# Optimization experiments

Measured on AMD Instinct MI355X. Metric: run time of the kernel, lower is better.

## Reference

```python
import jax, jax.numpy as jnp
import numpy as np
from functools import partial

TAU = 2.0
V_TH = 1.0
ALPHA = 2.0  # spikingjelly surrogate.ATan default alpha
EPS = 1e-5   # nn.LayerNorm default eps

@jax.custom_vjp
def atan_spike(v):
    # Heaviside forward; ATan surrogate gradient in bwd.
    return (v >= 0.0).astype(v.dtype)

def _atan_fwd(v):
    return atan_spike(v), v

def _atan_bwd(v, g):
    sg = (ALPHA / 2.0) / (1.0 + (jnp.pi / 2.0 * ALPHA * v) ** 2)
    return (g * sg,)

atan_spike.defvjp(_atan_fwd, _atan_bwd)

def lif_multi_step(x):
    # x: [B, T, H]; LIF with decay_input=True, v_reset=0 (hard reset), detach_reset=True.
    xt = jnp.swapaxes(x, 0, 1)  # [T, B, H]
    v0 = jnp.zeros(x.shape[:1] + x.shape[2:], dtype=x.dtype)  # reset_net per call
    def step(v, x_t):
        v = v + (x_t - v) / TAU            # charge
        s = atan_spike(v - V_TH)           # fire (surrogate grad)
        v = v * (1.0 - jax.lax.stop_gradient(s))  # hard reset to 0, detached spike
        return v, s
    _, spikes = jax.lax.scan(step, v0, xt)
    return jnp.swapaxes(spikes, 0, 1)  # [B, T, H]

def layer_norm(x, gamma, beta):
    mu = jnp.mean(x, axis=-1, keepdims=True)
    var = jnp.mean((x - mu) ** 2, axis=-1, keepdims=True)
    return (x - mu) * jax.lax.rsqrt(var + EPS) * gamma + beta

def setup_inputs() -> dict:
    key = jax.random.key(0)
    ks = jax.random.split(key, 5)
    B, T, D, H = 64, 1024, 256, 512
    x = jax.random.normal(ks[0], (B, T, D), dtype=jnp.float32)
    sc1 = 1.0 / np.sqrt(D)
    sc2 = 1.0 / np.sqrt(H)
    W1 = jax.random.uniform(ks[1], (H, D), jnp.float32, -sc1, sc1)
    b1 = jax.random.uniform(ks[2], (H,), jnp.float32, -sc1, sc1)
    W2 = jax.random.uniform(ks[3], (D, H), jnp.float32, -sc2, sc2)
    b2 = jax.random.uniform(ks[4], (D,), jnp.float32, -sc2, sc2)
    g1 = jnp.ones((H,), jnp.float32); be1 = jnp.zeros((H,), jnp.float32)
    g2 = jnp.ones((D,), jnp.float32); be2 = jnp.zeros((D,), jnp.float32)
    return {"x": x, "W1": W1, "b1": b1, "g1": g1, "be1": be1,
            "W2": W2, "b2": b2, "g2": g2, "be2": be2}

def reference(x, W1, b1, g1, be1, W2, b2, g2, be2):
    residual = x
    h = jnp.einsum('btd,hd->bth', x, W1) + b1   # fc1
    h = layer_norm(h, g1, be1)                   # norm1
    h = lif_multi_step(h)                        # lif1 (dropout = identity, eval)
    y = jnp.einsum('bth,dh->btd', h, W2) + b2    # fc2
    y = layer_norm(y, g2, be2)                   # norm2
    y = lif_multi_step(y)                        # lif2
    return residual + y
```

## Files before the change

### kernel.cpp

```cpp
#include <hip/hip_runtime.h>

typedef int   v4i __attribute__((ext_vector_type(4)));
typedef int  v16i __attribute__((ext_vector_type(16)));
typedef float v4f __attribute__((ext_vector_type(4)));

#define TT 1024
#define DD 256
#define HH 512
#define CB 32
#define CM (CB*TT)

static __device__ __forceinline__ double shfl_xor_d(double x, int m) {
    union { double d; int u[2]; } a; a.d = x;
    a.u[0] = __shfl_xor(a.u[0], m);
    a.u[1] = __shfl_xor(a.u[1], m);
    return a.d;
}

__global__ __launch_bounds__(256) void prep_w_k(const float* __restrict__ W1,
                                                const float* __restrict__ W2,
                                                signed char* __restrict__ W1p,
                                                signed char* __restrict__ W2p) {
    int i = blockIdx.x * 256 + threadIdx.x;
    {
        double a = (double)W1[i];
        double inv = 1024.0, s = 1.0 / 1024.0;
#pragma unroll
        for (int p = 0; p < 5; ++p) {
            int d = (int)(a * inv);
            a -= d * s;
            W1p[(size_t)p * 131072 + i] = (signed char)d;
            inv *= 128.0; s *= (1.0 / 128.0);
        }
    }
    {
        double a = (double)W2[i];
        double inv = 1024.0, s = 1.0 / 1024.0;
#pragma unroll
        for (int p = 0; p < 5; ++p) {
            int d = (int)(a * inv);
            a -= d * s;
            W2p[(size_t)p * 131072 + i] = (signed char)d;
            inv *= 128.0; s *= (1.0 / 128.0);
        }
    }
}

__global__ __launch_bounds__(256) void split_x_k(const float* __restrict__ xc,
                                                 signed char* __restrict__ Xp) {
    int gid = blockIdx.x * 256 + threadIdx.x;
    int e0 = gid * 4;
    v4f xv = *(const v4f*)(xc + e0);
    int dg[4][5];
#pragma unroll
    for (int e = 0; e < 4; ++e) {
        float a = xv[e];
        float inv = 8.0f, s = 0.125f;
#pragma unroll
        for (int p = 0; p < 5; ++p) {
            int d = (int)(a * inv);
            a -= (float)d * s;
            dg[e][p] = d;
            inv *= 128.0f; s *= (1.0f / 128.0f);
        }
    }
#pragma unroll
    for (int p = 0; p < 5; ++p) {
        int pk = (dg[0][p] & 255) | ((dg[1][p] & 255) << 8) |
                 ((dg[2][p] & 255) << 16) | ((dg[3][p] & 255) << 24);
        *(int*)(Xp + (size_t)p * ((size_t)CM * 256) + e0) = pk;
    }
}

__global__ __launch_bounds__(256, 2) void gemm1_i8(
    const signed char* __restrict__ Xp, const signed char* __restrict__ W1p,
    const float* __restrict__ b1, double* __restrict__ Hn,
    double* __restrict__ PS1w, double* __restrict__ PQ1w) {
    __shared__ signed char Asm[5 * 8192];

    const int tid = threadIdx.x;
    const int wn = tid >> 6, lane = tid & 63, lrow = lane & 31, lhalf = lane >> 5;
    const int ch = blockIdx.x;
    const int m0 = blockIdx.y * 32;

    {
        const int r = tid >> 3, k0 = (tid & 7) * 32;
        const int swz = (r & 15) << 4;
#pragma unroll
        for (int p = 0; p < 5; ++p) {
            const signed char* sp = Xp + (size_t)p * ((size_t)CM * 256) +
                                    (size_t)(m0 + r) * 256 + k0;
            v4i v0 = *(const v4i*)(sp);
            v4i v1 = *(const v4i*)(sp + 16);
            *(v4i*)&Asm[p * 8192 + r * 256 + (k0 ^ swz)] = v0;
            *(v4i*)&Asm[p * 8192 + r * 256 + ((k0 + 16) ^ swz)] = v1;
        }
    }

    const int colbase = ch * 256 + wn * 32 + lrow;
    const signed char* bptr = W1p + (size_t)colbase * 256 + lhalf * 16;

    v4i bf[3][5];
#pragma unroll
    for (int s = 0; s < 2; ++s)
#pragma unroll
        for (int j = 0; j < 5; ++j)
            bf[s][j] = *(const v4i*)(bptr + (size_t)j * 131072 +
                                     (s >> 3) * 32768 + (s & 7) * 32);

    v16i acc[5];

    __syncthreads();

    const double scl[5] = {0x1p-13, 0x1p-20, 0x1p-27, 0x1p-34, 0x1p-41};
    const int aswz = (lrow & 15) << 4;

#pragma unroll
    for (int p = 0; p < 2; ++p) {
#pragma unroll
        for (int g = 0; g < 5; ++g)
#pragma unroll
            for (int r = 0; r < 16; ++r) acc[g][r] = 0;
#pragma unroll
        for (int ksl = 0; ksl < 8; ++ksl) {
            const int s = p * 8 + ksl;
            if (s + 2 < 16) {
                const int s2 = s + 2;
#pragma unroll
                for (int j = 0; j < 5; ++j)
                    bf[s2 % 3][j] = *(const v4i*)(bptr + (size_t)j * 131072 +
                                                  (s2 >> 3) * 32768 + (s2 & 7) * 32);
            }
            v4i af[5];
#pragma unroll
            for (int i = 0; i < 5; ++i)
                af[i] = *(const v4i*)&Asm[i * 8192 + lrow * 256 +
                                          ((ksl * 32 + lhalf * 16) ^ aswz)];
#pragma unroll
            for (int j = 0; j < 5; ++j)
#pragma unroll
                for (int i = 0; i + j < 5; ++i)
                    acc[i + j] = __builtin_amdgcn_mfma_i32_32x32x32_i8(
                        af[i], bf[s % 3][j], acc[i + j], 0, 0, 0);
        }
        const int col = colbase + p * 128;
        const double bcol = (double)b1[col];
        const size_t qbase = (size_t)((ch * 2 + p) * 4 + wn) * CM + m0;
#pragma unroll
        for (int r = 0; r < 16; ++r) {
            double t = 0.0;
#pragma unroll
            for (int g = 0; g < 5; ++g) t = fma((double)acc[g][r], scl[g], t);
            const double hr = t + bcol;
            const int crow = (r & 3) + 8 * (r >> 2) + 4 * lhalf;
            Hn[(size_t)(m0 + crow) * HH + col] = hr;
            double ps = hr, pq = hr * hr;
#pragma unroll
            for (int m = 1; m < 32; m <<= 1) {
                ps += shfl_xor_d(ps, m);
                pq += shfl_xor_d(pq, m);
            }
            if (lrow == 0) {
                PS1w[qbase + crow] = ps;
                PQ1w[qbase + crow] = pq;
            }
        }
    }
}

__global__ __launch_bounds__(256) void stats1_fin(const double* __restrict__ PS1w,
                                                  const double* __restrict__ PQ1w,
                                                  double2* __restrict__ MUIV1) {
    int row = blockIdx.x * 256 + threadIdx.x;
    double S = 0.0, Q = 0.0;
#pragma unroll
    for (int q = 0; q < 16; ++q) {
        S += PS1w[(size_t)q * CM + row];
        Q += PQ1w[(size_t)q * CM + row];
    }
    double mu = S * (1.0 / 512.0);
    double var = Q * (1.0 / 512.0) - mu * mu;
    MUIV1[row] = make_double2(mu, 1.0 / sqrt(var + 1e-5));
}

__global__ __launch_bounds__(64) void lif1_k(const double* __restrict__ Hn,
                                             const double2* __restrict__ MUIV,
                                             const float* __restrict__ g1,
                                             const float* __restrict__ be1,
                                             signed char* __restrict__ S) {
    const int b = blockIdx.x >> 3;
    const int h = (blockIdx.x & 7) * 64 + threadIdx.x;
    __shared__ double2 MI[4][16];
    const double* src = Hn + (size_t)b * TT * HH + h;
    signed char* dst = S + (size_t)b * TT * HH + h;
    const double gg = (double)g1[h], be = (double)be1[h];
    if (threadIdx.x < 48)
        MI[threadIdx.x >> 4][threadIdx.x & 15] = MUIV[(size_t)b * TT + threadIdx.x];
    double buf[4][16];
#pragma unroll
    for (int gq = 0; gq < 3; ++gq)
#pragma unroll
        for (int t = 0; t < 16; ++t)
            buf[gq][t] = src[(size_t)(gq * 16 + t) * HH];
    __syncthreads();
    double v = 0.0;
    for (int g4 = 0; g4 < 64; g4 += 4) {
#pragma unroll
        for (int u = 0; u < 4; ++u) {
            const int g = g4 + u;
            __syncthreads();
            if (g + 3 < 64) {
                if (threadIdx.x < 16)
                    MI[(g + 3) & 3][threadIdx.x] =
                        MUIV[(size_t)b * TT + (g + 3) * 16 + threadIdx.x];
#pragma unroll
                for (int t = 0; t < 16; ++t)
                    buf[(u + 3) & 3][t] = src[(size_t)((g + 3) * 16 + t) * HH];
            }
#pragma unroll
            for (int t = 0; t < 16; ++t) {
                const double2 mi = MI[g & 3][t];
                const double x = (buf[u][t] - mi.x) * mi.y * gg + be;
                v += (x - v) * 0.5;
                const bool sp = (v >= 1.0);
                dst[(size_t)(g * 16 + t) * HH] = sp ? 1 : 0;
                if (sp) v = 0.0;
            }
        }
    }
}

__global__ __launch_bounds__(256, 2) void gemm2_i8(
    const signed char* __restrict__ Sb, const signed char* __restrict__ W2p,
    const float* __restrict__ b2, double* __restrict__ Yn,
    double2* __restrict__ MUIV2) {
    __shared__ signed char Asm[32 * 512];
    __shared__ double RSs[2][4][32], RQs[2][4][32];

    const int tid = threadIdx.x;
    const int wn = tid >> 6, lane = tid & 63, lrow = lane & 31, lhalf = lane >> 5;
    const int m0 = blockIdx.x * 32;

    {
        const int r = tid >> 3, k0 = (tid & 7) * 64;
        const signed char* sp = Sb + (size_t)(m0 + r) * HH + k0;
        const int swz = (r & 15) << 4;
#pragma unroll
        for (int q = 0; q < 4; ++q) {
            v4i v = *(const v4i*)(sp + q * 16);
            *(v4i*)&Asm[r * 512 + ((k0 + q * 16) ^ swz)] = v;
        }
    }

    const signed char* bptr = W2p + (size_t)(wn * 32 + lrow) * 512 + lhalf * 16;

    v4i bf[3][5];
#pragma unroll
    for (int s = 0; s < 2; ++s)
#pragma unroll
        for (int j = 0; j < 5; ++j)
            bf[s][j] = *(const v4i*)(bptr + (size_t)j * 131072 +
                                     (s >> 4) * 65536 + (s & 15) * 32);

    v16i acc[5];

    __syncthreads();

    const double scl[5] = {0x1p-10, 0x1p-17, 0x1p-24, 0x1p-31, 0x1p-38};
    const int aswz = (lrow & 15) << 4;

#pragma unroll
    for (int p = 0; p < 2; ++p) {
#pragma unroll
        for (int g = 0; g < 5; ++g)
#pragma unroll
            for (int r = 0; r < 16; ++r) acc[g][r] = 0;
#pragma unroll
        for (int ksl = 0; ksl < 16; ++ksl) {
            const int s = p * 16 + ksl;
            if (s + 2 < 32) {
                const int s2 = s + 2;
#pragma unroll
                for (int j = 0; j < 5; ++j)
                    bf[s2 % 3][j] = *(const v4i*)(bptr + (size_t)j * 131072 +
                                                  (s2 >> 4) * 65536 + (s2 & 15) * 32);
            }
            v4i a = *(const v4i*)&Asm[lrow * 512 + ((ksl * 32 + lhalf * 16) ^ aswz)];
#pragma unroll
            for (int j = 0; j < 5; ++j)
                acc[j] = __builtin_amdgcn_mfma_i32_32x32x32_i8(a, bf[s % 3][j], acc[j], 0, 0, 0);
        }
        const int col = p * 128 + wn * 32 + lrow;
        const double bcol = (double)b2[col];
#pragma unroll
        for (int r = 0; r < 16; ++r) {
            double t = 0.0;
#pragma unroll
            for (int g = 0; g < 5; ++g) t = fma((double)acc[g][r], scl[g], t);
            const double yr = t + bcol;
            const int crow = (r & 3) + 8 * (r >> 2) + 4 * lhalf;
            Yn[(size_t)(m0 + crow) * DD + col] = yr;
            double ps = yr, pq = yr * yr;
#pragma unroll
            for (int m = 1; m < 32; m <<= 1) {
                ps += shfl_xor_d(ps, m);
                pq += shfl_xor_d(pq, m);
            }
            if (lrow == 0) {
                RSs[p][wn][crow] = ps;
                RQs[p][wn][crow] = pq;
            }
        }
    }
    __syncthreads();
    if (tid < 32) {
        double Ssum = 0.0, Qsum = 0.0;
#pragma unroll
        for (int p = 0; p < 2; ++p)
#pragma unroll
            for (int w = 0; w < 4; ++w) { Ssum += RSs[p][w][tid]; Qsum += RQs[p][w][tid]; }
        const double mu = Ssum * (1.0 / 256.0);
        const double var = Qsum * (1.0 / 256.0) - mu * mu;
        MUIV2[m0 + tid] = make_double2(mu, 1.0 / sqrt(var + 1e-5));
    }
}

__global__ __launch_bounds__(64) void lif2_k(const double* __restrict__ Yn,
                                             const double2* __restrict__ MUIV,
                                             const float* __restrict__ g2,
                                             const float* __restrict__ be2,
                                             const float* __restrict__ X,
                                             float* __restrict__ out) {
    const int b = blockIdx.x >> 2;
    const int d = (blockIdx.x & 3) * 64 + threadIdx.x;
    __shared__ double2 MI[4][16];
    const double* src = Yn + (size_t)b * TT * DD + d;
    const float* xs = X + (size_t)b * TT * DD + d;
    float* dst = out + (size_t)b * TT * DD + d;
    const double gg = (double)g2[d], be = (double)be2[d];
    if (threadIdx.x < 48)
        MI[threadIdx.x >> 4][threadIdx.x & 15] = MUIV[(size_t)b * TT + threadIdx.x];
    double bufy[4][16];
    float bufx[4][16];
#pragma unroll
    for (int gq = 0; gq < 3; ++gq)
#pragma unroll
        for (int t = 0; t < 16; ++t) {
            bufy[gq][t] = src[(size_t)(gq * 16 + t) * DD];
            bufx[gq][t] = xs[(size_t)(gq * 16 + t) * DD];
        }
    __syncthreads();
    double v = 0.0;
    for (int g4 = 0; g4 < 64; g4 += 4) {
#pragma unroll
        for (int u = 0; u < 4; ++u) {
            const int g = g4 + u;
            __syncthreads();
            if (g + 3 < 64) {
                if (threadIdx.x < 16)
                    MI[(g + 3) & 3][threadIdx.x] =
                        MUIV[(size_t)b * TT + (g + 3) * 16 + threadIdx.x];
#pragma unroll
                for (int t = 0; t < 16; ++t) {
                    bufy[(u + 3) & 3][t] = src[(size_t)((g + 3) * 16 + t) * DD];
                    bufx[(u + 3) & 3][t] = xs[(size_t)((g + 3) * 16 + t) * DD];
                }
            }
#pragma unroll
            for (int t = 0; t < 16; ++t) {
                const double2 mi = MI[g & 3][t];
                const double x = (bufy[u][t] - mi.x) * mi.y * gg + be;
                v += (x - v) * 0.5;
                const bool sp = (v >= 1.0);
                __builtin_nontemporal_store(bufx[u][t] + (sp ? 1.0f : 0.0f),
                                            &dst[(size_t)(g * 16 + t) * DD]);
                if (sp) v = 0.0;
            }
        }
    }
}

extern "C" void kernel_launch(void* const* d_in, const int* in_sizes, int n_in,
                              void* d_out, int out_size, void* d_ws, size_t ws_size,
                              hipStream_t stream) {
    const float* x   = (const float*)d_in[0];
    const float* W1  = (const float*)d_in[1];
    const float* b1  = (const float*)d_in[2];
    const float* g1  = (const float*)d_in[3];
    const float* be1 = (const float*)d_in[4];
    const float* W2  = (const float*)d_in[5];
    const float* b2  = (const float*)d_in[6];
    const float* g2  = (const float*)d_in[7];
    const float* be2 = (const float*)d_in[8];
    float* out = (float*)d_out;

    char* ws = (char*)d_ws;
    signed char* W1p = (signed char*)ws;
    signed char* W2p = (signed char*)(ws + (1ull << 20));
    double*      Hn  = (double*)(ws + (2ull << 20));
    signed char* Sb  = (signed char*)(ws + (130ull << 20));
    double*      Yn  = (double*)(ws + (146ull << 20));
    signed char* Xp    = (signed char*)(ws + (146ull << 20));
    double*      PS1w  = (double*)(ws + (186ull << 20));
    double*      PQ1w  = (double*)(ws + (190ull << 20));
    double2*     MUIV1 = (double2*)(ws + (194ull << 20));
    double2*     MUIV2 = (double2*)(ws + (210ull << 20));

    prep_w_k<<<dim3(512), dim3(256), 0, stream>>>(W1, W2, W1p, W2p);

    for (int c = 0; c < 2; ++c) {
        const float* xc = x + (size_t)c * CM * DD;
        float* outc = out + (size_t)c * CM * DD;
        split_x_k<<<dim3(8192), dim3(256), 0, stream>>>(xc, Xp);
        gemm1_i8<<<dim3(2, CM / 32), dim3(256), 0, stream>>>(Xp, W1p, b1, Hn, PS1w, PQ1w);
        stats1_fin<<<dim3(CM / 256), dim3(256), 0, stream>>>(PS1w, PQ1w, MUIV1);
        lif1_k<<<dim3(CB * 8), dim3(64), 0, stream>>>(Hn, MUIV1, g1, be1, Sb);
        gemm2_i8<<<dim3(CM / 32), dim3(256), 0, stream>>>(Sb, W2p, b2, Yn, MUIV2);
        lif2_k<<<dim3(CB * 4), dim3(64), 0, stream>>>(Yn, MUIV2, g2, be2, xc, outc);
    }
}
```

Before: 715.2 us.

## Fuse x digit split into gemm1 and switch GEMMs to 16x16x64 int8 MFMA

The separate split_x_k kernel is removed. gemm1 now loads fp32 x directly and decomposes it into five int8 digit planes in shared memory, so the 5-plane int8 staging buffer no longer makes a round trip through global memory. Both GEMMs move from 32x32x32 to 16x16x64 int8 MFMA with a 2x2 wave layout. Each block now covers all output columns in a loop over phases, and gemm1 becomes a one-dimensional grid. gemm2's in-block LayerNorm stat reduction is replaced by partial sums plus a new stats2_fin kernel, and workspace buffers are remapped. The cost is one extra launch and redundant digit splitting, since each gemm1 block now handles all 512 columns.

```diff
diff --git a/kernel.cpp b/kernel.cpp
--- a/kernel.cpp
+++ b/kernel.cpp
@@ -1,7 +1,6 @@
 #include <hip/hip_runtime.h>
 
 typedef int   v4i __attribute__((ext_vector_type(4)));
-typedef int  v16i __attribute__((ext_vector_type(16)));
 typedef float v4f __attribute__((ext_vector_type(4)));
 
 #define TT 1024
@@ -46,123 +45,122 @@
     }
 }
 
-__global__ __launch_bounds__(256) void split_x_k(const float* __restrict__ xc,
-                                                 signed char* __restrict__ Xp) {
-    int gid = blockIdx.x * 256 + threadIdx.x;
-    int e0 = gid * 4;
-    v4f xv = *(const v4f*)(xc + e0);
-    int dg[4][5];
-#pragma unroll
-    for (int e = 0; e < 4; ++e) {
-        float a = xv[e];
-        float inv = 8.0f, s = 0.125f;
-#pragma unroll
-        for (int p = 0; p < 5; ++p) {
-            int d = (int)(a * inv);
-            a -= (float)d * s;
-            dg[e][p] = d;
-            inv *= 128.0f; s *= (1.0f / 128.0f);
-        }
-    }
-#pragma unroll
-    for (int p = 0; p < 5; ++p) {
-        int pk = (dg[0][p] & 255) | ((dg[1][p] & 255) << 8) |
-                 ((dg[2][p] & 255) << 16) | ((dg[3][p] & 255) << 24);
-        *(int*)(Xp + (size_t)p * ((size_t)CM * 256) + e0) = pk;
-    }
-}
-
 __global__ __launch_bounds__(256, 2) void gemm1_i8(
-    const signed char* __restrict__ Xp, const signed char* __restrict__ W1p,
+    const float* __restrict__ X, const signed char* __restrict__ W1p,
     const float* __restrict__ b1, double* __restrict__ Hn,
     double* __restrict__ PS1w, double* __restrict__ PQ1w) {
     __shared__ signed char Asm[5 * 8192];
 
     const int tid = threadIdx.x;
-    const int wn = tid >> 6, lane = tid & 63, lrow = lane & 31, lhalf = lane >> 5;
-    const int ch = blockIdx.x;
-    const int m0 = blockIdx.y * 32;
+    const int wave = tid >> 6, lane = tid & 63;
+    const int wm = wave >> 1, wn = wave & 1;
+    const int lcol = lane & 15, lq = lane >> 4;
+    const int m0 = blockIdx.x * 32;
 
     {
         const int r = tid >> 3, k0 = (tid & 7) * 32;
+        const float* xp = X + (size_t)(m0 + r) * DD + k0;
         const int swz = (r & 15) << 4;
 #pragma unroll
-        for (int p = 0; p < 5; ++p) {
-            const signed char* sp = Xp + (size_t)p * ((size_t)CM * 256) +
-                                    (size_t)(m0 + r) * 256 + k0;
-            v4i v0 = *(const v4i*)(sp);
-            v4i v1 = *(const v4i*)(sp + 16);
-            *(v4i*)&Asm[p * 8192 + r * 256 + (k0 ^ swz)] = v0;
-            *(v4i*)&Asm[p * 8192 + r * 256 + ((k0 + 16) ^ swz)] = v1;
-        }
-    }
-
-    const int colbase = ch * 256 + wn * 32 + lrow;
-    const signed char* bptr = W1p + (size_t)colbase * 256 + lhalf * 16;
-
-    v4i bf[3][5];
-#pragma unroll
-    for (int s = 0; s < 2; ++s)
-#pragma unroll
-        for (int j = 0; j < 5; ++j)
-            bf[s][j] = *(const v4i*)(bptr + (size_t)j * 131072 +
-                                     (s >> 3) * 32768 + (s & 7) * 32);
-
-    v16i acc[5];
+        for (int half = 0; half < 2; ++half) {
+            float xe[16];
+#pragma unroll
+            for (int q = 0; q < 4; ++q)
+                *(v4f*)(xe + q * 4) = *(const v4f*)(xp + half * 16 + q * 4);
+            int pk[5][4];
+#pragma unroll
+            for (int q = 0; q < 4; ++q)
+#pragma unroll
+                for (int e = 0; e < 4; ++e) {
+                    float a = xe[q * 4 + e];
+                    float inv = 8.0f, s = 0.125f;
+#pragma unroll
+                    for (int p = 0; p < 5; ++p) {
+                        int dg = (int)(a * inv);
+                        a -= (float)dg * s;
+                        int byte = (dg & 255) << (8 * e);
+                        if (e == 0) pk[p][q] = byte; else pk[p][q] |= byte;
+                        inv *= 128.0f; s *= (1.0f / 128.0f);
+                    }
+                }
+#pragma unroll
+            for (int p = 0; p < 5; ++p)
+                *(v4i*)&Asm[p * 8192 + r * 256 + ((k0 + half * 16) ^ swz)] =
+                    *(const v4i*)&pk[p][0];
+        }
+    }
+
+    const signed char* bptr = W1p + (size_t)(wn * 16 + lcol) * 256 + lq * 16;
+
+    v4i bf[2][5];
+#pragma unroll
+    for (int j = 0; j < 5; ++j)
+        bf[0][j] = *(const v4i*)(bptr + (size_t)j * 131072);
 
     __syncthreads();
 
     const double scl[5] = {0x1p-13, 0x1p-20, 0x1p-27, 0x1p-34, 0x1p-41};
-    const int aswz = (lrow & 15) << 4;
-
-#pragma unroll
-    for (int p = 0; p < 2; ++p) {
+    const int arow = wm * 16 + lcol;
+    const int abase = arow * 256;
+    const int aswz = lcol << 4;
+
+#pragma unroll 1
+    for (int ph = 0; ph < 16; ++ph) {
+        v4i acc[5];
 #pragma unroll
         for (int g = 0; g < 5; ++g)
 #pragma unroll
-            for (int r = 0; r < 16; ++r) acc[g][r] = 0;
-#pragma unroll
-        for (int ksl = 0; ksl < 8; ++ksl) {
-            const int s = p * 8 + ksl;
-            if (s + 2 < 16) {
-                const int s2 = s + 2;
+            for (int r = 0; r < 4; ++r) acc[g][r] = 0;
+
+#pragma unroll
+        for (int ks = 0; ks < 4; ++ks) {
+            if (ks != 3 || ph != 15) {
+                const int s1 = ph * 4 + ks + 1;
+                const size_t off = (size_t)(s1 >> 2) * 8192 + (size_t)((ks + 1) & 3) * 64;
 #pragma unroll
                 for (int j = 0; j < 5; ++j)
-                    bf[s2 % 3][j] = *(const v4i*)(bptr + (size_t)j * 131072 +
-                                                  (s2 >> 3) * 32768 + (s2 & 7) * 32);
+                    bf[(ks + 1) & 1][j] = *(const v4i*)(bptr + (size_t)j * 131072 + off);
             }
             v4i af[5];
 #pragma unroll
             for (int i = 0; i < 5; ++i)
-                af[i] = *(const v4i*)&Asm[i * 8192 + lrow * 256 +
-                                          ((ksl * 32 + lhalf * 16) ^ aswz)];
+                af[i] = *(const v4i*)&Asm[i * 8192 + abase +
+                                          ((ks * 64 + lq * 16) ^ aswz)];
 #pragma unroll
             for (int j = 0; j < 5; ++j)
 #pragma unroll
                 for (int i = 0; i + j < 5; ++i)
-                    acc[i + j] = __builtin_amdgcn_mfma_i32_32x32x32_i8(
-                        af[i], bf[s % 3][j], acc[i + j], 0, 0, 0);
-        }
-        const int col = colbase + p * 128;
+                    acc[i + j] = __builtin_amdgcn_mfma_i32_16x16x64_i8(
+                        af[i], bf[ks & 1][j], acc[i + j], 0, 0, 0);
+        }
+
+        const int col = ph * 32 + wn * 16 + lcol;
         const double bcol = (double)b1[col];
-        const size_t qbase = (size_t)((ch * 2 + p) * 4 + wn) * CM + m0;
-#pragma unroll
-        for (int r = 0; r < 16; ++r) {
+        double vv[4], ps[4], pq[4];
+#pragma unroll
+        for (int r = 0; r < 4; ++r) {
             double t = 0.0;
 #pragma unroll
             for (int g = 0; g < 5; ++g) t = fma((double)acc[g][r], scl[g], t);
-            const double hr = t + bcol;
-            const int crow = (r & 3) + 8 * (r >> 2) + 4 * lhalf;
-            Hn[(size_t)(m0 + crow) * HH + col] = hr;
-            double ps = hr, pq = hr * hr;
-#pragma unroll
-            for (int m = 1; m < 32; m <<= 1) {
-                ps += shfl_xor_d(ps, m);
-                pq += shfl_xor_d(pq, m);
-            }
-            if (lrow == 0) {
-                PS1w[qbase + crow] = ps;
-                PQ1w[qbase + crow] = pq;
+            vv[r] = t + bcol;
+            ps[r] = vv[r]; pq[r] = vv[r] * vv[r];
+        }
+#pragma unroll
+        for (int m = 1; m < 16; m <<= 1)
+#pragma unroll
+            for (int r = 0; r < 4; ++r) {
+                ps[r] += shfl_xor_d(ps[r], m);
+                pq[r] += shfl_xor_d(pq[r], m);
+            }
+#pragma unroll
+        for (int r = 0; r < 4; ++r)
+            Hn[(size_t)(m0 + wm * 16 + lq * 4 + r) * HH + col] = vv[r];
+        if (lcol == 0) {
+            const size_t qb = (size_t)(ph * 2 + wn) * CM + m0 + wm * 16 + lq * 4;
+#pragma unroll
+            for (int r = 0; r < 4; ++r) {
+                PS1w[qb + r] = ps[r];
+                PQ1w[qb + r] = pq[r];
             }
         }
     }
@@ -174,7 +172,7 @@
     int row = blockIdx.x * 256 + threadIdx.x;
     double S = 0.0, Q = 0.0;
 #pragma unroll
-    for (int q = 0; q < 16; ++q) {
+    for (int q = 0; q < 32; ++q) {
         S += PS1w[(size_t)q * CM + row];
         Q += PQ1w[(size_t)q * CM + row];
     }
@@ -233,12 +231,13 @@
 __global__ __launch_bounds__(256, 2) void gemm2_i8(
     const signed char* __restrict__ Sb, const signed char* __restrict__ W2p,
     const float* __restrict__ b2, double* __restrict__ Yn,
-    double2* __restrict__ MUIV2) {
+    double* __restrict__ PS2w, double* __restrict__ PQ2w) {
     __shared__ signed char Asm[32 * 512];
-    __shared__ double RSs[2][4][32], RQs[2][4][32];
 
     const int tid = threadIdx.x;
-    const int wn = tid >> 6, lane = tid & 63, lrow = lane & 31, lhalf = lane >> 5;
+    const int wave = tid >> 6, lane = tid & 63;
+    const int wm = wave >> 1, wn = wave & 1;
+    const int lcol = lane & 15, lq = lane >> 4;
     const int m0 = blockIdx.x * 32;
 
     {
@@ -252,77 +251,89 @@
         }
     }
 
-    const signed char* bptr = W2p + (size_t)(wn * 32 + lrow) * 512 + lhalf * 16;
-
-    v4i bf[3][5];
-#pragma unroll
-    for (int s = 0; s < 2; ++s)
-#pragma unroll
-        for (int j = 0; j < 5; ++j)
-            bf[s][j] = *(const v4i*)(bptr + (size_t)j * 131072 +
-                                     (s >> 4) * 65536 + (s & 15) * 32);
-
-    v16i acc[5];
+    const signed char* bptr = W2p + (size_t)(wn * 16 + lcol) * 512 + lq * 16;
+
+    v4i bf[2][5];
+#pragma unroll
+    for (int j = 0; j < 5; ++j)
+        bf[0][j] = *(const v4i*)(bptr + (size_t)j * 131072);
 
     __syncthreads();
 
     const double scl[5] = {0x1p-10, 0x1p-17, 0x1p-24, 0x1p-31, 0x1p-38};
-    const int aswz = (lrow & 15) << 4;
-
-#pragma unroll
-    for (int p = 0; p < 2; ++p) {
+    const int arow = wm * 16 + lcol;
+    const int abase = arow * 512;
+    const int aswz = lcol << 4;
+
+#pragma unroll 1
+    for (int ph = 0; ph < 8; ++ph) {
+        v4i acc[5];
 #pragma unroll
         for (int g = 0; g < 5; ++g)
 #pragma unroll
-            for (int r = 0; r < 16; ++r) acc[g][r] = 0;
-#pragma unroll
-        for (int ksl = 0; ksl < 16; ++ksl) {
-            const int s = p * 16 + ksl;
-            if (s + 2 < 32) {
-                const int s2 = s + 2;
+            for (int r = 0; r < 4; ++r) acc[g][r] = 0;
+
+#pragma unroll
+        for (int ks = 0; ks < 8; ++ks) {
+            if (ks != 7 || ph != 7) {
+                const int s1 = ph * 8 + ks + 1;
+                const size_t off = (size_t)(s1 >> 3) * 16384 + (size_t)((ks + 1) & 7) * 64;
 #pragma unroll
                 for (int j = 0; j < 5; ++j)
-                    bf[s2 % 3][j] = *(const v4i*)(bptr + (size_t)j * 131072 +
-                                                  (s2 >> 4) * 65536 + (s2 & 15) * 32);
-            }
-            v4i a = *(const v4i*)&Asm[lrow * 512 + ((ksl * 32 + lhalf * 16) ^ aswz)];
+                    bf[(ks + 1) & 1][j] = *(const v4i*)(bptr + (size_t)j * 131072 + off);
+            }
+            v4i a = *(const v4i*)&Asm[abase + ((ks * 64 + lq * 16) ^ aswz)];
 #pragma unroll
             for (int j = 0; j < 5; ++j)
-                acc[j] = __builtin_amdgcn_mfma_i32_32x32x32_i8(a, bf[s % 3][j], acc[j], 0, 0, 0);
-        }
-        const int col = p * 128 + wn * 32 + lrow;
+                acc[j] = __builtin_amdgcn_mfma_i32_16x16x64_i8(
+                    a, bf[ks & 1][j], acc[j], 0, 0, 0);
+        }
+
+        const int col = ph * 32 + wn * 16 + lcol;
         const double bcol = (double)b2[col];
-#pragma unroll
-        for (int r = 0; r < 16; ++r) {
+        double vv[4], ps[4], pq[4];
+#pragma unroll
+        for (int r = 0; r < 4; ++r) {
             double t = 0.0;
 #pragma unroll
             for (int g = 0; g < 5; ++g) t = fma((double)acc[g][r], scl[g], t);
-            const double yr = t + bcol;
-            const int crow = (r & 3) + 8 * (r >> 2) + 4 * lhalf;
-            Yn[(size_t)(m0 + crow) * DD + col] = yr;
-            double ps = yr, pq = yr * yr;
-#pragma unroll
-            for (int m = 1; m < 32; m <<= 1) {
-                ps += shfl_xor_d(ps, m);
-                pq += shfl_xor_d(pq, m);
-            }
-            if (lrow == 0) {
-                RSs[p][wn][crow] = ps;
-                RQs[p][wn][crow] = pq;
-            }
-        }
-    }
-    __syncthreads();
-    if (tid < 32) {
-        double Ssum = 0.0, Qsum = 0.0;
-#pragma unroll
-        for (int p = 0; p < 2; ++p)
-#pragma unroll
-            for (int w = 0; w < 4; ++w) { Ssum += RSs[p][w][tid]; Qsum += RQs[p][w][tid]; }
-        const double mu = Ssum * (1.0 / 256.0);
-        const double var = Qsum * (1.0 / 256.0) - mu * mu;
-        MUIV2[m0 + tid] = make_double2(mu, 1.0 / sqrt(var + 1e-5));
-    }
+            vv[r] = t + bcol;
+            ps[r] = vv[r]; pq[r] = vv[r] * vv[r];
+        }
+#pragma unroll
+        for (int m = 1; m < 16; m <<= 1)
+#pragma unroll
+            for (int r = 0; r < 4; ++r) {
+                ps[r] += shfl_xor_d(ps[r], m);
+                pq[r] += shfl_xor_d(pq[r], m);
+            }
+#pragma unroll
+        for (int r = 0; r < 4; ++r)
+            Yn[(size_t)(m0 + wm * 16 + lq * 4 + r) * DD + col] = vv[r];
+        if (lcol == 0) {
+            const size_t qb = (size_t)(ph * 2 + wn) * CM + m0 + wm * 16 + lq * 4;
+#pragma unroll
+            for (int r = 0; r < 4; ++r) {
+                PS2w[qb + r] = ps[r];
+                PQ2w[qb + r] = pq[r];
+            }
+        }
+    }
+}
+
+__global__ __launch_bounds__(256) void stats2_fin(const double* __restrict__ PS2w,
+                                                  const double* __restrict__ PQ2w,
+                                                  double2* __restrict__ MUIV2) {
+    int row = blockIdx.x * 256 + threadIdx.x;
+    double S = 0.0, Q = 0.0;
+#pragma unroll
+    for (int q = 0; q < 16; ++q) {
+        S += PS2w[(size_t)q * CM + row];
+        Q += PQ2w[(size_t)q * CM + row];
+    }
+    double mu = S * (1.0 / 256.0);
+    double var = Q * (1.0 / 256.0) - mu * mu;
+    MUIV2[row] = make_double2(mu, 1.0 / sqrt(var + 1e-5));
 }
 
 __global__ __launch_bounds__(64) void lif2_k(const double* __restrict__ Yn,
@@ -400,22 +411,23 @@
     double*      Hn  = (double*)(ws + (2ull << 20));
     signed char* Sb  = (signed char*)(ws + (130ull << 20));
     double*      Yn  = (double*)(ws + (146ull << 20));
-    signed char* Xp    = (signed char*)(ws + (146ull << 20));
-    double*      PS1w  = (double*)(ws + (186ull << 20));
-    double*      PQ1w  = (double*)(ws + (190ull << 20));
-    double2*     MUIV1 = (double2*)(ws + (194ull << 20));
-    double2*     MUIV2 = (double2*)(ws + (210ull << 20));
+    double*      PS1w  = (double*)(ws + (146ull << 20));
+    double*      PQ1w  = (double*)(ws + (154ull << 20));
+    double2*     MUIV1 = (double2*)(ws + (162ull << 20));
+    double*      PS2w  = (double*)(ws + (2ull << 20));
+    double*      PQ2w  = (double*)(ws + (6ull << 20));
+    double2*     MUIV2 = (double2*)(ws + (10ull << 20));
 
     prep_w_k<<<dim3(512), dim3(256), 0, stream>>>(W1, W2, W1p, W2p);
 
     for (int c = 0; c < 2; ++c) {
         const float* xc = x + (size_t)c * CM * DD;
         float* outc = out + (size_t)c * CM * DD;
-        split_x_k<<<dim3(8192), dim3(256), 0, stream>>>(xc, Xp);
-        gemm1_i8<<<dim3(2, CM / 32), dim3(256), 0, stream>>>(Xp, W1p, b1, Hn, PS1w, PQ1w);
+        gemm1_i8<<<dim3(CM / 32), dim3(256), 0, stream>>>(xc, W1p, b1, Hn, PS1w, PQ1w);
         stats1_fin<<<dim3(CM / 256), dim3(256), 0, stream>>>(PS1w, PQ1w, MUIV1);
         lif1_k<<<dim3(CB * 8), dim3(64), 0, stream>>>(Hn, MUIV1, g1, be1, Sb);
-        gemm2_i8<<<dim3(CM / 32), dim3(256), 0, stream>>>(Sb, W2p, b2, Yn, MUIV2);
+        gemm2_i8<<<dim3(CM / 32), dim3(256), 0, stream>>>(Sb, W2p, b2, Yn, PS2w, PQ2w);
+        stats2_fin<<<dim3(CM / 256), dim3(256), 0, stream>>>(PS2w, PQ2w, MUIV2);
         lif2_k<<<dim3(CB * 4), dim3(64), 0, stream>>>(Yn, MUIV2, g2, be2, xc, outc);
     }
 }
```

New measurement: 896.4 us. 25.3% more time.
